# Kernel tuning notes

Hardware: AMD Instinct MI355X
Metric: run time of the kernel (lower is better)

Reference implementation:

```python
import jax, jax.numpy as jnp
import numpy as np
import math

B, C, D, H, W = 1, 64, 16, 16, 16
HEADS = 4
HD = C // HEADS  # head_dim = 16


def conv3d(x, w, b, pad):
    # x: [B,C,D,H,W], w: [O,I,kd,kh,kw], pad: (pd,ph,pw)
    y = jax.lax.conv_general_dilated(
        x, w, window_strides=(1, 1, 1),
        padding=[(p, p) for p in pad],
        dimension_numbers=('NCDHW', 'OIDHW', 'NCDHW'))
    return y + b[None, :, None, None, None]


def setup_inputs() -> dict:
    key = jax.random.key(0)
    ks = jax.random.split(key, 10)
    s = 0.02
    return {
        'x': jax.random.normal(ks[0], (B, C, D, H, W), jnp.float32),
        'gamma': jax.random.normal(ks[1], (1,), jnp.float32),
        'w_sp': jax.random.normal(ks[2], (C, C, 1, 3, 3), jnp.float32) * s,
        'b_sp': jax.random.normal(ks[3], (C,), jnp.float32) * s,
        'w_spec': jax.random.normal(ks[4], (C, C, 3, 1, 1), jnp.float32) * s,
        'b_spec': jax.random.normal(ks[5], (C,), jnp.float32) * s,
        'w_qkv': jax.random.normal(ks[6], (3 * C, C, 1, 1, 1), jnp.float32) * s,
        'b_qkv': jax.random.normal(ks[7], (3 * C,), jnp.float32) * s,
        'w_proj': jax.random.normal(ks[8], (C, C, 1, 1, 1), jnp.float32) * s,
        'b_proj': jax.random.normal(ks[9], (C,), jnp.float32) * s,
    }


def _decay_exponent(dtype):
    # Faithful to the torch permute quirk (requires H == W):
    # exponent[i,j,k,m,n,o] = |i-m| + |j-k| + |n-o|
    dd = jnp.abs(jnp.arange(D)[:, None] - jnp.arange(D)[None, :]).astype(dtype)  # [D,D]
    hh = jnp.abs(jnp.arange(H)[:, None] - jnp.arange(H)[None, :]).astype(dtype)  # [H,H]
    ww = jnp.abs(jnp.arange(W)[:, None] - jnp.arange(W)[None, :]).astype(dtype)  # [W,W]
    return (dd[:, None, None, :, None, None]      # i (axis0), m (axis3)
            + hh[None, :, :, None, None, None]    # j (axis1), k (axis2)
            + ww[None, None, None, None, :, :])   # n (axis4), o (axis5)


def _forward(x, gamma, w_sp, b_sp, w_spec, b_spec, w_qkv, b_qkv, w_proj, b_proj):
    x = conv3d(x, w_sp, b_sp, (0, 1, 1))
    x = conv3d(x, w_spec, b_spec, (1, 0, 0))
    qkv = conv3d(x, w_qkv, b_qkv, (0, 0, 0))
    q, k, v = jnp.split(qkv, 3, axis=1)
    rs = lambda t: t.reshape(B, HEADS, HD, D, H, W)
    q, k, v = rs(q), rs(k), rs(v)

    g = jax.nn.sigmoid(gamma[0])
    decay = g ** _decay_exponent(x.dtype)  # [D,H,W,D,W,W] (H==W)

    # attn[b,h,i,j,k,m,n,o]: (i,j,k)=query D,H,W ; (m,n,o)=key D,H,W
    attn = jnp.einsum('bhdijk,bhdmno->bhijkmno', q, k) / math.sqrt(HD)
    attn = jax.nn.softmax(attn * decay, axis=-1)  # softmax over key-W axis o only
    out = jnp.einsum('bhijkmno,bhdmno->bhdijk', attn, v)
    out = out.reshape(B, C, D, H, W)
    return conv3d(out, w_proj, b_proj, (0, 0, 0))


def reference(x, gamma, w_sp, b_sp, w_spec, b_spec, w_qkv, b_qkv, w_proj, b_proj):
    return _forward(x, gamma, w_sp, b_sp, w_spec, b_spec, w_qkv, b_qkv, w_proj, b_proj)
```

## Files before the change

kernel.cpp:

```cpp
#include <hip/hip_runtime.h>
#include <math.h>

#define CN   262144
#define BTP 196
#define PTP 68

typedef __attribute__((ext_vector_type(8))) short short8;
typedef __attribute__((ext_vector_type(4))) short short4v;
typedef __attribute__((ext_vector_type(4))) float float4v;

static __device__ __forceinline__ unsigned short f2bf(float f) {
    union { float f; unsigned u; } v; v.f = f;
    unsigned r = (v.u + 0x7FFFu + ((v.u >> 16) & 1u)) >> 16;
    return (unsigned short)r;
}

__global__ __launch_bounds__(256, 4) void conv_sp_wfuse_kernel(
        const float* __restrict__ x, const float* __restrict__ w_sp,
        const float* __restrict__ b_sp, float* __restrict__ y1,
        const float* __restrict__ w_spec, const float* __restrict__ b_spec,
        const float* __restrict__ w_qkv, const float* __restrict__ b_qkv,
        unsigned short* __restrict__ wfb, float* __restrict__ bfv) {
    int tid = threadIdx.x;
    if (blockIdx.x >= 256) {
        int idx = (blockIdx.x - 256) * 256 + tid;
        int oc = idx / 192;
        int r  = idx % 192;
        float s = 0.f;
        #pragma unroll 8
        for (int ci = 0; ci < 64; ++ci)
            s += w_qkv[oc * 64 + ci] * w_spec[ci * 192 + r];
        if (oc < 64) s *= 0.25f;
        wfb[oc * 192 + r] = f2bf(s);
        if (idx < 192) {
            float t = b_qkv[idx];
            for (int ci = 0; ci < 64; ++ci) t += w_qkv[idx * 64 + ci] * b_spec[ci];
            if (idx < 64) t *= 0.25f;
            bfv[idx] = t;
        }
        return;
    }
    __shared__ __align__(16) unsigned short Bt[16 * BTP];
    int d = blockIdx.x >> 4;
    int h = blockIdx.x & 15;
    int px = tid & 15, cig = tid >> 4;

    float rcur[12], rnxt[12];
    #define LOAD_CHUNK(dh_, rr)                                            \
        {                                                                  \
            int hh = h + (dh_) - 1;                                        \
            _Pragma("unroll")                                              \
            for (int cc = 0; cc < 4; ++cc) {                               \
                int ci = cig * 4 + cc;                                     \
                const float* xr = x + ci * 4096 + d * 256 + hh * 16;       \
                _Pragma("unroll")                                          \
                for (int dw = 0; dw < 3; ++dw) {                           \
                    int ww = px + dw - 1;                                  \
                    float v = 0.f;                                         \
                    if (hh >= 0 && hh <= 15 && ww >= 0 && ww <= 15)        \
                        v = xr[ww];                                        \
                    (rr)[cc * 3 + dw] = v;                                 \
                }                                                          \
            }                                                              \
        }

    LOAD_CHUNK(0, rcur);

    int wv = tid >> 6, lane = tid & 63;
    int quad = lane >> 4, l15 = lane & 15;
    int co = wv * 16 + l15;
    float4v czero = {0.f, 0.f, 0.f, 0.f};
    float4v acc = czero;

    #pragma unroll
    for (int c = 0; c < 3; ++c) {
        __syncthreads();
        #pragma unroll
        for (int cc = 0; cc < 4; ++cc) {
            int ci = cig * 4 + cc;
            Bt[px * BTP +       ci] = f2bf(rcur[cc * 3 + 0]);
            Bt[px * BTP +  64 + ci] = f2bf(rcur[cc * 3 + 1]);
            Bt[px * BTP + 128 + ci] = f2bf(rcur[cc * 3 + 2]);
        }
        __syncthreads();
        if (c < 2) LOAD_CHUNK(c + 1, rnxt);

        const unsigned short* brow = Bt + l15 * BTP + quad * 8;
        #pragma unroll
        for (int ks = 0; ks < 6; ++ks) {
            int k0 = ks * 32 + quad * 8;
            const float* wr = w_sp + co * 576 + (k0 & 63) * 9 + c * 3 + (k0 >> 6);
            short8 af;
            #pragma unroll
            for (int jj = 0; jj < 8; ++jj) af[jj] = (short)f2bf(wr[jj * 9]);
            short4v lo = *(const short4v*)(brow + ks * 32);
            short4v hi = *(const short4v*)(brow + ks * 32 + 4);
            short8 bf8 = {lo[0], lo[1], lo[2], lo[3], hi[0], hi[1], hi[2], hi[3]};
            acc = __builtin_amdgcn_mfma_f32_16x16x32_bf16(af, bf8, acc, 0, 0, 0);
        }
        #pragma unroll
        for (int q2 = 0; q2 < 12; ++q2) rcur[q2] = rnxt[q2];
    }

    int p = d * 256 + h * 16 + l15;
    #pragma unroll
    for (int r = 0; r < 4; ++r) {
        int coo = wv * 16 + quad * 4 + r;
        y1[coo * 4096 + p] = acc[r] + b_sp[coo];
    }
    #undef LOAD_CHUNK
}

__global__ __launch_bounds__(512, 4) void qkv_mfma_kernel(
        const float* __restrict__ y1, const unsigned short* __restrict__ wfb,
        const float* __restrict__ bfv,
        unsigned short* __restrict__ qb, unsigned short* __restrict__ kb,
        unsigned short* __restrict__ vtb) {
    __shared__ __align__(16) unsigned short Bt[32 * BTP];
    int bI  = blockIdx.x;
    int ocg = bI % 3;
    int pq  = (bI / 3) & 7;
    int d   = bI / 24;
    int tid = threadIdx.x;

    {
        int px  = tid & 31;
        int cig = tid >> 5;
        const float* yb = y1 + d * 256 + pq * 32 + px;
        #pragma unroll
        for (int cc = 0; cc < 4; ++cc) {
            int ci = cig * 4 + cc;
            const float* yc = yb + ci * 4096;
            #pragma unroll
            for (int t = 0; t < 3; ++t) {
                float v = 0.f;
                if (!((d == 0 && t == 0) || (d == 15 && t == 2)))
                    v = yc[(t - 1) * 256];
                Bt[px * BTP + ci * 3 + t] = f2bf(v);
            }
        }
    }

    int wv = tid >> 6, lane = tid & 63;
    int quad = lane >> 4, l15 = lane & 15;
    int Mt = wv >> 1;
    int nt = wv & 1;

    short8 af[6];
    {
        const unsigned short* ab = wfb + (ocg * 64 + Mt * 16 + l15) * 192 + quad * 8;
        #pragma unroll
        for (int ks = 0; ks < 6; ++ks) af[ks] = *(const short8*)(ab + ks * 32);
    }
    float bias[4];
    #pragma unroll
    for (int r = 0; r < 4; ++r) bias[r] = bfv[ocg * 64 + Mt * 16 + quad * 4 + r];

    __syncthreads();

    float4v czero = {0.f, 0.f, 0.f, 0.f};
    float4v acc = czero;
    {
        const unsigned short* brow = Bt + (nt * 16 + l15) * BTP + quad * 8;
        #pragma unroll
        for (int ks = 0; ks < 6; ++ks) {
            short4v lo = *(const short4v*)(brow + ks * 32);
            short4v hi = *(const short4v*)(brow + ks * 32 + 4);
            short8 bf8 = {lo[0], lo[1], lo[2], lo[3], hi[0], hi[1], hi[2], hi[3]};
            acc = __builtin_amdgcn_mfma_f32_16x16x32_bf16(af[ks], bf8, acc, 0, 0, 0);
        }
    }

    {
        int p = d * 256 + pq * 32 + nt * 16 + l15;
        if (ocg == 2) {
            int h = (p >> 4) & 15, w0 = p & 15;
            int kap = 8 * (w0 >> 2) + 4 * (h & 1) + (w0 & 3);
            unsigned short* dst = vtb + ((Mt * 16 + d) * 8 + (h >> 1)) * 512
                                      + (quad * 4) * 32 + kap;
            #pragma unroll
            for (int r = 0; r < 4; ++r) dst[r * 32] = f2bf(acc[r] + bias[r]);
        } else {
            unsigned short* dst = (ocg == 0 ? qb : kb) + Mt * 65536 + p * 16 + quad * 4;
            unsigned t0 = (unsigned)f2bf(acc[0] + bias[0])
                        | ((unsigned)f2bf(acc[1] + bias[1]) << 16);
            unsigned t1 = (unsigned)f2bf(acc[2] + bias[2])
                        | ((unsigned)f2bf(acc[3] + bias[3]) << 16);
            *(unsigned*)dst = t0;
            *(unsigned*)(dst + 2) = t1;
        }
    }
}

__global__ __launch_bounds__(512, 4) void attn_kernel(
        const unsigned short* __restrict__ qb, const unsigned short* __restrict__ kb,
        const unsigned short* __restrict__ vtb, const float* __restrict__ gamma,
        float* __restrict__ aoall) {
    __shared__ __align__(16) unsigned short ksh[2][4096];
    __shared__ __align__(16) unsigned short vsh[2][4096];
    __shared__ float gp[32];
    int tid = threadIdx.x;
    int bI = blockIdx.x;
    int head = bI >> 8;
    int mg   = (bI >> 5) & 7;
    int oct  = bI & 31;

    if (tid < 32) {
        float g = 1.f / (1.f + __expf(-gamma[0]));
        gp[tid] = __powf(g, (float)tid);
    }

    int wv = tid >> 6, lane = tid & 63;
    int quad = lane >> 4, l15 = lane & 15;
    int t = oct * 8 + wv;
    int i = t >> 4, j = t & 15;

    short8 zero8 = {0, 0, 0, 0, 0, 0, 0, 0};
    float4v czero = {0.f, 0.f, 0.f, 0.f};
    short8 qf = zero8;
    if (quad < 2)
        qf = *(const short8*)(qb + head * 65536 + (t * 16 + l15) * 16 + quad * 8);

    const unsigned short* kbh = kb  + head * 65536 + mg * 2 * 4096;
    const unsigned short* vbh = vtb + head * 65536 + mg * 2 * 4096;
    float4 k0 = ((const float4*)kbh)[tid];
    float4 v0 = ((const float4*)vbh)[tid];
    float4 k1 = ((const float4*)(kbh + 4096))[tid];
    float4 v1 = ((const float4*)(vbh + 4096))[tid];
    ((float4*)ksh[0])[tid] = k0;
    ((float4*)vsh[0])[tid] = v0;
    ((float4*)ksh[1])[tid] = k1;
    ((float4*)vsh[1])[tid] = v1;
    __syncthreads();

    float wd[4];
    #pragma unroll
    for (int r = 0; r < 4; ++r)
        wd[r] = gp[abs(l15 - (quad * 4 + r))] * 1.4426950408889634f;

    float4v O = czero;
    #pragma unroll
    for (int mm = 0; mm < 2; ++mm) {
        int m = mg * 2 + mm;
        const unsigned short* kk = ksh[mm];
        const unsigned short* vv = vsh[mm];
        int eim = abs(i - m);
        #pragma unroll
        for (int np = 0; np < 8; ++np) {
            union { unsigned u[4]; short8 s8; } a2u;
            #pragma unroll
            for (int s = 0; s < 2; ++s) {
                int n = np * 2 + s;
                short8 a1 = zero8;
                if (quad < 2)
                    a1 = *(const short8*)(kk + n * 256 + l15 * 16 + quad * 8);
                float4v d1 = __builtin_amdgcn_mfma_f32_16x16x32_bf16(a1, qf, czero, 0, 0, 0);
                float smn = gp[eim + abs(j - n)];
                float e0 = __builtin_amdgcn_exp2f(d1[0] * smn * wd[0]);
                float e1 = __builtin_amdgcn_exp2f(d1[1] * smn * wd[1]);
                float e2 = __builtin_amdgcn_exp2f(d1[2] * smn * wd[2]);
                float e3 = __builtin_amdgcn_exp2f(d1[3] * smn * wd[3]);
                float sm = e0 + e1 + e2 + e3;
                sm += __shfl_xor(sm, 16);
                sm += __shfl_xor(sm, 32);
                float inv = __builtin_amdgcn_rcpf(sm);
                union { float f; unsigned u; } p0, p1, p2, p3;
                p0.f = e0 * inv; p1.f = e1 * inv;
                p2.f = e2 * inv; p3.f = e3 * inv;
                a2u.u[s * 2]     = ((p0.u + 0x8000u) >> 16) | ((p1.u + 0x8000u) & 0xFFFF0000u);
                a2u.u[s * 2 + 1] = ((p2.u + 0x8000u) >> 16) | ((p3.u + 0x8000u) & 0xFFFF0000u);
            }
            short8 b2 = *(const short8*)(vv + np * 512 + l15 * 32 + quad * 8);
            O = __builtin_amdgcn_mfma_f32_16x16x32_bf16(a2u.s8, b2, O, 0, 0, 0);
        }
    }

    float* aop = aoall + mg * CN;
    float4 ov = {O[0], O[1], O[2], O[3]};
    *(float4*)(aop + (head * 16 + l15) * 4096 + t * 16 + quad * 4) = ov;
}

__global__ __launch_bounds__(256, 8) void proj_mfma_kernel(
        const float* __restrict__ aoall,
        const float* __restrict__ w, const float* __restrict__ b,
        float* __restrict__ out) {
    __shared__ __align__(16) unsigned short Bt[16 * PTP];
    int d   = blockIdx.x >> 4;
    int p16 = blockIdx.x & 15;
    int tid = threadIdx.x;

    {
        int px = tid & 15, cig = tid >> 4;
        int gbase = d * 256 + p16 * 16 + px;
        #pragma unroll
        for (int cc = 0; cc < 4; ++cc) {
            int ci = cig * 4 + cc;
            int ga = ci * 4096 + gbase;
            float v = 0.f;
            #pragma unroll
            for (int k = 0; k < 8; ++k) v += aoall[k * CN + ga];
            Bt[px * PTP + ci] = f2bf(v);
        }
    }
    __syncthreads();

    int wv = tid >> 6, lane = tid & 63;
    int quad = lane >> 4, l15 = lane & 15;
    float4v czero = {0.f, 0.f, 0.f, 0.f};
    float4v acc = czero;

    short8 af[2];
    const float* wsrc = w + (wv * 16 + l15) * 64 + quad * 8;
    #pragma unroll
    for (int ks = 0; ks < 2; ++ks) {
        float4 wa = *(const float4*)(wsrc + ks * 32);
        float4 wb = *(const float4*)(wsrc + ks * 32 + 4);
        short8 a8 = {(short)f2bf(wa.x), (short)f2bf(wa.y), (short)f2bf(wa.z),
                     (short)f2bf(wa.w), (short)f2bf(wb.x), (short)f2bf(wb.y),
                     (short)f2bf(wb.z), (short)f2bf(wb.w)};
        af[ks] = a8;
    }
    const unsigned short* brow = Bt + l15 * PTP + quad * 8;
    #pragma unroll
    for (int ks = 0; ks < 2; ++ks) {
        short4v lo = *(const short4v*)(brow + ks * 32);
        short4v hi = *(const short4v*)(brow + ks * 32 + 4);
        short8 bf8 = {lo[0], lo[1], lo[2], lo[3], hi[0], hi[1], hi[2], hi[3]};
        acc = __builtin_amdgcn_mfma_f32_16x16x32_bf16(af[ks], bf8, acc, 0, 0, 0);
    }

    int p = d * 256 + p16 * 16 + l15;
    #pragma unroll
    for (int r = 0; r < 4; ++r) {
        int oc = wv * 16 + quad * 4 + r;
        out[oc * 4096 + p] = acc[r] + b[oc];
    }
}

extern "C" void kernel_launch(void* const* d_in, const int* in_sizes, int n_in,
                              void* d_out, int out_size, void* d_ws, size_t ws_size,
                              hipStream_t stream) {
    const float* x      = (const float*)d_in[0];
    const float* gamma  = (const float*)d_in[1];
    const float* w_sp   = (const float*)d_in[2];
    const float* b_sp   = (const float*)d_in[3];
    const float* w_spec = (const float*)d_in[4];
    const float* b_spec = (const float*)d_in[5];
    const float* w_qkv  = (const float*)d_in[6];
    const float* b_qkv  = (const float*)d_in[7];
    const float* w_proj = (const float*)d_in[8];
    const float* b_proj = (const float*)d_in[9];
    float* out = (float*)d_out;

    float* ws = (float*)d_ws;
    float* y1  = ws;
    unsigned short* wfb = (unsigned short*)(ws + CN);
    float* bfv = ws + CN + 20480;
    unsigned short* qb  = (unsigned short*)(ws + 2 * CN);
    unsigned short* kb  = (unsigned short*)(ws + 2 * CN + CN / 2);
    unsigned short* vtb = (unsigned short*)(ws + 3 * CN);
    float* aoall = ws + 3 * CN + CN / 2;

    conv_sp_wfuse_kernel<<< 400, 256, 0, stream>>>(x, w_sp, b_sp, y1,
                                                   w_spec, b_spec, w_qkv, b_qkv,
                                                   wfb, bfv);
    qkv_mfma_kernel     <<< 384, 512, 0, stream>>>(y1, wfb, bfv, qb, kb, vtb);
    attn_kernel         <<<1024, 512, 0, stream>>>(qb, kb, vtb, gamma, aoall);
    proj_mfma_kernel    <<< 256, 256, 0, stream>>>(aoall, w_proj, b_proj, out);
}
```

Baseline: 119.0 us.

## Fuse output projection into attention kernel via per-head MFMA and atomic accumulation

Removes the separate projection kernel and the 8-way partial-output buffer. Each attention wave now stages its 16x16 output tile in shared memory as bf16 and multiplies it by the matching 16-column slice of w_proj with MFMA. It accumulates into the zeroed output with float atomicAdd, adding the bias once from head 0, key-group 0. It also packs the bf16 probabilities with a byte-permute instead of shift/mask. The trade is one fewer launch and no partial-sum round trip through memory, against a memset plus 32 contending atomic adds per output element (4 heads × 8 key groups) and non-deterministic summation order.

```diff
diff --git a/kernel.cpp b/kernel.cpp
--- a/kernel.cpp
+++ b/kernel.cpp
@@ -3,7 +3,6 @@
 
 #define CN   262144
 #define BTP 196
-#define PTP 68
 
 typedef __attribute__((ext_vector_type(8))) short short8;
 typedef __attribute__((ext_vector_type(4))) short short4v;
@@ -192,12 +191,14 @@
     }
 }
 
-__global__ __launch_bounds__(512, 4) void attn_kernel(
+__global__ __launch_bounds__(512, 4) void attn_proj_kernel(
         const unsigned short* __restrict__ qb, const unsigned short* __restrict__ kb,
         const unsigned short* __restrict__ vtb, const float* __restrict__ gamma,
-        float* __restrict__ aoall) {
+        const float* __restrict__ w_proj, const float* __restrict__ b_proj,
+        float* __restrict__ out) {
     __shared__ __align__(16) unsigned short ksh[2][4096];
     __shared__ __align__(16) unsigned short vsh[2][4096];
+    __shared__ __align__(16) unsigned short osh_all[8 * 16 * 24];
     __shared__ float gp[32];
     int tid = threadIdx.x;
     int bI = blockIdx.x;
@@ -267,73 +268,43 @@
                 union { float f; unsigned u; } p0, p1, p2, p3;
                 p0.f = e0 * inv; p1.f = e1 * inv;
                 p2.f = e2 * inv; p3.f = e3 * inv;
-                a2u.u[s * 2]     = ((p0.u + 0x8000u) >> 16) | ((p1.u + 0x8000u) & 0xFFFF0000u);
-                a2u.u[s * 2 + 1] = ((p2.u + 0x8000u) >> 16) | ((p3.u + 0x8000u) & 0xFFFF0000u);
+                a2u.u[s * 2]     = __builtin_amdgcn_perm(p1.u + 0x8000u, p0.u + 0x8000u, 0x07060302u);
+                a2u.u[s * 2 + 1] = __builtin_amdgcn_perm(p3.u + 0x8000u, p2.u + 0x8000u, 0x07060302u);
             }
             short8 b2 = *(const short8*)(vv + np * 512 + l15 * 32 + quad * 8);
             O = __builtin_amdgcn_mfma_f32_16x16x32_bf16(a2u.s8, b2, O, 0, 0, 0);
         }
     }
 
-    float* aop = aoall + mg * CN;
-    float4 ov = {O[0], O[1], O[2], O[3]};
-    *(float4*)(aop + (head * 16 + l15) * 4096 + t * 16 + quad * 4) = ov;
-}
-
-__global__ __launch_bounds__(256, 8) void proj_mfma_kernel(
-        const float* __restrict__ aoall,
-        const float* __restrict__ w, const float* __restrict__ b,
-        float* __restrict__ out) {
-    __shared__ __align__(16) unsigned short Bt[16 * PTP];
-    int d   = blockIdx.x >> 4;
-    int p16 = blockIdx.x & 15;
-    int tid = threadIdx.x;
-
-    {
-        int px = tid & 15, cig = tid >> 4;
-        int gbase = d * 256 + p16 * 16 + px;
-        #pragma unroll
-        for (int cc = 0; cc < 4; ++cc) {
-            int ci = cig * 4 + cc;
-            int ga = ci * 4096 + gbase;
-            float v = 0.f;
-            #pragma unroll
-            for (int k = 0; k < 8; ++k) v += aoall[k * CN + ga];
-            Bt[px * PTP + ci] = f2bf(v);
-        }
-    }
-    __syncthreads();
-
-    int wv = tid >> 6, lane = tid & 63;
-    int quad = lane >> 4, l15 = lane & 15;
-    float4v czero = {0.f, 0.f, 0.f, 0.f};
-    float4v acc = czero;
-
-    short8 af[2];
-    const float* wsrc = w + (wv * 16 + l15) * 64 + quad * 8;
-    #pragma unroll
-    for (int ks = 0; ks < 2; ++ks) {
-        float4 wa = *(const float4*)(wsrc + ks * 32);
-        float4 wb = *(const float4*)(wsrc + ks * 32 + 4);
-        short8 a8 = {(short)f2bf(wa.x), (short)f2bf(wa.y), (short)f2bf(wa.z),
-                     (short)f2bf(wa.w), (short)f2bf(wb.x), (short)f2bf(wb.y),
-                     (short)f2bf(wb.z), (short)f2bf(wb.w)};
-        af[ks] = a8;
-    }
-    const unsigned short* brow = Bt + l15 * PTP + quad * 8;
-    #pragma unroll
-    for (int ks = 0; ks < 2; ++ks) {
-        short4v lo = *(const short4v*)(brow + ks * 32);
-        short4v hi = *(const short4v*)(brow + ks * 32 + 4);
-        short8 bf8 = {lo[0], lo[1], lo[2], lo[3], hi[0], hi[1], hi[2], hi[3]};
-        acc = __builtin_amdgcn_mfma_f32_16x16x32_bf16(af[ks], bf8, acc, 0, 0, 0);
-    }
-
-    int p = d * 256 + p16 * 16 + l15;
-    #pragma unroll
-    for (int r = 0; r < 4; ++r) {
-        int oc = wv * 16 + quad * 4 + r;
-        out[oc * 4096 + p] = acc[r] + b[oc];
+    unsigned short* osh = osh_all + wv * 384;
+    #pragma unroll
+    for (int r = 0; r < 4; ++r)
+        osh[(quad * 4 + r) * 24 + l15] = f2bf(O[r]);
+    short8 b_o = zero8;
+    if (quad < 2)
+        b_o = *(const short8*)(osh + l15 * 24 + quad * 8);
+
+    bool addb = (head == 0) && (mg == 0);
+    #pragma unroll
+    for (int Mt2 = 0; Mt2 < 4; ++Mt2) {
+        short8 a_wp = zero8;
+        if (quad < 2) {
+            const float* wr = w_proj + (Mt2 * 16 + l15) * 64 + head * 16 + quad * 8;
+            float4 wa = *(const float4*)wr;
+            float4 wb = *(const float4*)(wr + 4);
+            a_wp[0] = (short)f2bf(wa.x); a_wp[1] = (short)f2bf(wa.y);
+            a_wp[2] = (short)f2bf(wa.z); a_wp[3] = (short)f2bf(wa.w);
+            a_wp[4] = (short)f2bf(wb.x); a_wp[5] = (short)f2bf(wb.y);
+            a_wp[6] = (short)f2bf(wb.z); a_wp[7] = (short)f2bf(wb.w);
+        }
+        float4v accp = __builtin_amdgcn_mfma_f32_16x16x32_bf16(a_wp, b_o, czero, 0, 0, 0);
+        #pragma unroll
+        for (int r = 0; r < 4; ++r) {
+            int oc = Mt2 * 16 + quad * 4 + r;
+            float val = accp[r];
+            if (addb) val += b_proj[oc];
+            atomicAdd(out + oc * 4096 + t * 16 + l15, val);
+        }
     }
 }
 
@@ -359,12 +330,12 @@
     unsigned short* qb  = (unsigned short*)(ws + 2 * CN);
     unsigned short* kb  = (unsigned short*)(ws + 2 * CN + CN / 2);
     unsigned short* vtb = (unsigned short*)(ws + 3 * CN);
-    float* aoall = ws + 3 * CN + CN / 2;
-
+
+    hipMemsetAsync(out, 0, (size_t)out_size * sizeof(float), stream);
     conv_sp_wfuse_kernel<<< 400, 256, 0, stream>>>(x, w_sp, b_sp, y1,
                                                    w_spec, b_spec, w_qkv, b_qkv,
                                                    wfb, bfv);
     qkv_mfma_kernel     <<< 384, 512, 0, stream>>>(y1, wfb, bfv, qb, kb, vtb);
-    attn_kernel         <<<1024, 512, 0, stream>>>(qb, kb, vtb, gamma, aoall);
-    proj_mfma_kernel    <<< 256, 256, 0, stream>>>(aoall, w_proj, b_proj, out);
-}
+    attn_proj_kernel    <<<1024, 512, 0, stream>>>(qb, kb, vtb, gamma,
+                                                   w_proj, b_proj, out);
+}
```

Result: slower. 126.1 us (+6.0%).
